# Kernel optimization log

Hardware: AMD Instinct MI355X
Metric: run time of the kernel (lower is better)

## Reference

```python
import jax, jax.numpy as jnp
import numpy as np

UNITS = 1024
NUM_HEADS = 8


def setup_inputs() -> dict:
    key = jax.random.key(0)
    k1, k2, k3 = jax.random.split(key, 3)
    B, S = 8, 1024
    memory = jax.random.normal(k1, (B, S, 2 * UNITS), dtype=jnp.float32)
    query = jax.random.normal(k2, (B, S, UNITS), dtype=jnp.float32)
    seq_mask = jax.random.randint(k3, (B, S), 0, 2, dtype=jnp.int32)
    b = jnp.zeros((1,), dtype=jnp.float32)  # learned scalar bias added to logits
    return {"memory": memory, "query": query, "seq_mask": seq_mask, "b": b}


def _split_heads(x, n):
    # [B, S, D] -> [B, n, S, D//n]
    B, S, D = x.shape
    return x.reshape(B, S, n, D // n).transpose(0, 2, 1, 3)


def reference(memory, query, seq_mask, b):
    H = NUM_HEADS
    depth = UNITS // H
    Q = _split_heads(query, H) * (depth ** -0.5)          # [B,H,S,d]
    k_mem, v_mem = jnp.split(memory, 2, axis=2)
    K = _split_heads(k_mem, H)                            # [B,H,S,d]
    V = _split_heads(v_mem, H)                            # [B,H,S,d]
    logits = jnp.einsum('bhqd,bhkd->bhqk', Q, K) + b[0]   # [B,H,S,S]
    mask = seq_mask.astype(jnp.float32)[:, None, None, :]  # [B,1,1,S]
    logits = logits + (-1e30) * (1.0 - mask)
    weights = jax.nn.softmax(logits, axis=-1)
    out = jnp.einsum('bhqk,bhkd->bhqd', weights, V)       # [B,H,S,d]
    B, _, S, _ = out.shape
    return out.transpose(0, 2, 1, 3).reshape(B, S, UNITS)
```

## Files before the change

### kernel.cpp

```cpp
#include <hip/hip_runtime.h>
#include <stdint.h>


typedef __attribute__((ext_vector_type(8))) short bf16x8;
typedef __attribute__((ext_vector_type(4))) float f32x4;
typedef __attribute__((ext_vector_type(16))) float f32x16;
typedef __attribute__((ext_vector_type(4))) unsigned int u32x4;

#define NB 8
#define SS 1024
#define NH 8
#define DH 128
#define BM 128
#define BN 64
#define KPAD 136
#define VPAD 72
#define NT (SS / BN)

__device__ __forceinline__ unsigned short f2bf(float f) {
    unsigned int u = __builtin_bit_cast(unsigned int, f);
    u += 0x7fffu + ((u >> 16) & 1u);
    return (unsigned short)(u >> 16);
}

__device__ __forceinline__ unsigned int cvt_pk_bf16(float lo, float hi) {
#if __has_builtin(__builtin_amdgcn_cvt_pk_bf16_f32)
    typedef __attribute__((ext_vector_type(2))) __bf16 bf16x2_t;
    bf16x2_t r = __builtin_amdgcn_cvt_pk_bf16_f32(lo, hi);
    return __builtin_bit_cast(unsigned int, r);
#else
    return (unsigned int)f2bf(lo) | ((unsigned int)f2bf(hi) << 16);
#endif
}

__device__ __forceinline__ void bar_lgkm() {
    asm volatile("s_waitcnt lgkmcnt(0)" ::: "memory");
    __builtin_amdgcn_s_barrier();
    asm volatile("" ::: "memory");
}

__device__ __forceinline__ void pswap(unsigned int &a, unsigned int &b) {
#if __has_builtin(__builtin_amdgcn_permlane32_swap)
    auto r = __builtin_amdgcn_permlane32_swap(a, b, false, false);
    a = (unsigned int)r[0];
    b = (unsigned int)r[1];
#else
    unsigned int sa = (unsigned int)__shfl_xor((int)a, 32, 64);
    unsigned int sb = (unsigned int)__shfl_xor((int)b, 32, 64);
    const bool hh = (threadIdx.x & 32) != 0;
    unsigned int na = hh ? sb : a;
    unsigned int nb = hh ? b : sa;
    a = na; b = nb;
#endif
}

__global__ __launch_bounds__(512, 4)
void attn_flash(const float* __restrict__ mem,
                const float* __restrict__ query,
                const int* __restrict__ seq_mask,
                float* __restrict__ out)
{
    __shared__ unsigned short K_lds[BN * KPAD];
    __shared__ unsigned short Vt_lds[DH * VPAD];

    const int tid  = threadIdx.x;
    const int wave = tid >> 6;
    const int lane = tid & 63;
    const int hi   = lane >> 5;
    const int l31  = lane & 31;
    const int wq   = wave & 3;
    const int wd   = wave >> 2;

    const int bh = blockIdx.x;
    const int b  = bh >> 3;
    const int h  = bh & 7;
    const int q0w = blockIdx.y * BM + wq * 32;

    bf16x8 qf[8];
    {
        const float* qb = query + ((size_t)(b * SS + q0w + l31) << 10) + h * DH + hi * 8;
        #pragma unroll
        for (int dep = 0; dep < 8; ++dep) {
            f32x4 lo = *(const f32x4*)(qb + dep * 16);
            f32x4 ho = *(const f32x4*)(qb + dep * 16 + 4);
            u32x4 q;
            q[0] = cvt_pk_bf16(lo[0], lo[1]);
            q[1] = cvt_pk_bf16(lo[2], lo[3]);
            q[2] = cvt_pk_bf16(ho[0], ho[1]);
            q[3] = cvt_pk_bf16(ho[2], ho[3]);
            qf[dep] = __builtin_bit_cast(bf16x8, q);
        }
    }

    f32x16 acc[2];
    #pragma unroll
    for (int dt = 0; dt < 2; ++dt)
        #pragma unroll
        for (int i = 0; i < 16; ++i) acc[dt][i] = 0.f;
    float l_i = 0.f;

    const float cs = 0.12752789747141537f;

    const int krow = tid >> 3;
    const int kcc  = (tid & 7) * 16;
    const int vq   = tid & 31;
    const int vg8  = tid >> 5;

    const float* kbase = mem + ((size_t)(b * SS) << 11) + h * DH;
    const float* vbase = kbase + 1024;
    const int* mbase = seq_mask + b * SS;

    int mv_cur = mbase[lane];
    int mv_nxt;

    for (int kt = 0; kt < NT; ++kt) {
        const int kk0 = kt * BN;

        bar_lgkm();

        {
            const float* src = kbase + ((size_t)(kk0 + krow) << 11) + kcc;
            f32x4 a0 = *(const f32x4*)src;
            f32x4 a1 = *(const f32x4*)(src + 4);
            f32x4 a2 = *(const f32x4*)(src + 8);
            f32x4 a3 = *(const f32x4*)(src + 12);
            u32x4 t0, t1;
            t0[0] = cvt_pk_bf16(a0[0], a0[1]);
            t0[1] = cvt_pk_bf16(a0[2], a0[3]);
            t0[2] = cvt_pk_bf16(a1[0], a1[1]);
            t0[3] = cvt_pk_bf16(a1[2], a1[3]);
            t1[0] = cvt_pk_bf16(a2[0], a2[1]);
            t1[1] = cvt_pk_bf16(a2[2], a2[3]);
            t1[2] = cvt_pk_bf16(a3[0], a3[1]);
            t1[3] = cvt_pk_bf16(a3[2], a3[3]);
            *(u32x4*)&K_lds[krow * KPAD + kcc] = t0;
            *(u32x4*)&K_lds[krow * KPAD + kcc + 8] = t1;
        }
        {
            const int d0 = vg8 * 8;
            const float* pa = vbase + ((size_t)(kk0 + 2 * vq) << 11) + d0;
            f32x4 a0 = *(const f32x4*)pa;
            f32x4 a1 = *(const f32x4*)(pa + 4);
            f32x4 b0 = *(const f32x4*)(pa + 2048);
            f32x4 b1 = *(const f32x4*)(pa + 2048 + 4);
            #pragma unroll
            for (int j = 0; j < 8; ++j) {
                float av = (j < 4) ? a0[j] : a1[j - 4];
                float bv = (j < 4) ? b0[j] : b1[j - 4];
                *(unsigned int*)&Vt_lds[(d0 + j) * VPAD + 2 * vq] =
                    cvt_pk_bf16(av, bv);
            }
        }

        const int kkn = (kt < NT - 1) ? kk0 + BN : kk0;
        mv_nxt = mbase[kkn + lane];

        bar_lgkm();

        const unsigned long long bmask = __ballot(mv_cur != 0);
        const unsigned int wsh0 = (unsigned int)(bmask >> (4 * hi));
        const unsigned int wsh1 = (unsigned int)(bmask >> (32 + 4 * hi));

        #pragma unroll
        for (int jt = 0; jt < 2; ++jt) {
            const unsigned int mword = jt ? wsh1 : wsh0;

            f32x16 s;
            #pragma unroll
            for (int i = 0; i < 16; ++i) s[i] = 0.f;
            __builtin_amdgcn_s_setprio(1);
            #pragma unroll
            for (int dep = 0; dep < 8; ++dep) {
                bf16x8 kf = *(const bf16x8*)&K_lds[(jt * 32 + l31) * KPAD + dep * 16 + hi * 8];
                s = __builtin_amdgcn_mfma_f32_32x32x16_bf16(kf, qf[dep], s, 0, 0, 0);
            }
            __builtin_amdgcn_s_setprio(0);

            float p[16];
            #pragma unroll
            for (int r = 0; r < 16; ++r) {
                const int sr = (r & 3) + 8 * (r >> 2);
                float e = __builtin_amdgcn_exp2f(s[r] * cs);
                p[r] = e * (float)((mword >> sr) & 1u);
            }
            {
                float t0 = (p[0] + p[1]) + (p[2] + p[3]);
                float t1 = (p[4] + p[5]) + (p[6] + p[7]);
                float t2 = (p[8] + p[9]) + (p[10] + p[11]);
                float t3 = (p[12] + p[13]) + (p[14] + p[15]);
                l_i += (t0 + t1) + (t2 + t3);
            }

            unsigned int w[8];
            #pragma unroll
            for (int i = 0; i < 8; ++i) w[i] = cvt_pk_bf16(p[2 * i], p[2 * i + 1]);
            pswap(w[0], w[2]); pswap(w[1], w[3]);
            pswap(w[4], w[6]); pswap(w[5], w[7]);
            bf16x8 af0 = __builtin_bit_cast(bf16x8, (u32x4){w[0], w[1], w[2], w[3]});
            bf16x8 af1 = __builtin_bit_cast(bf16x8, (u32x4){w[4], w[5], w[6], w[7]});

            __builtin_amdgcn_s_setprio(1);
            #pragma unroll
            for (int ksl = 0; ksl < 2; ++ksl) {
                bf16x8 ap = ksl ? af1 : af0;
                #pragma unroll
                for (int dt = 0; dt < 2; ++dt) {
                    bf16x8 bv = *(const bf16x8*)&Vt_lds[((wd * 2 + dt) * 32 + l31) * VPAD +
                                                        jt * 32 + ksl * 16 + hi * 8];
                    acc[dt] = __builtin_amdgcn_mfma_f32_32x32x16_bf16(ap, bv, acc[dt], 0, 0, 0);
                }
            }
            __builtin_amdgcn_s_setprio(0);
        }

        mv_cur = mv_nxt;
    }

    float lt = l_i + __shfl_xor(l_i, 32, 64);
    float invl = 1.f / lt;
    #pragma unroll
    for (int r = 0; r < 16; ++r) {
        const int qrow = (r & 3) + 8 * (r >> 2) + 4 * hi;
        float iv = __shfl(invl, qrow, 64);
        float* ob = out + ((size_t)(b * SS + q0w + qrow) << 10) + h * DH + wd * 64 + l31;
        ob[0]  = acc[0][r] * iv;
        ob[32] = acc[1][r] * iv;
    }
}

extern "C" void kernel_launch(void* const* d_in, const int* in_sizes, int n_in,
                              void* d_out, int out_size, void* d_ws, size_t ws_size,
                              hipStream_t stream)
{
    (void)in_sizes; (void)n_in; (void)d_ws; (void)ws_size; (void)out_size;
    const float* mem    = (const float*)d_in[0];
    const float* query  = (const float*)d_in[1];
    const int* seq_mask = (const int*)d_in[2];
    dim3 grid(NB * NH, SS / BM);
    attn_flash<<<grid, 512, 0, stream>>>(mem, query, seq_mask, (float*)d_out);
}
```

Baseline: 197.1 us.

## Split QK^T key columns across paired waves and exchange P through LDS

Before, each of the two waves sharing a query tile computed the full 64-key QK^T and softmax, duplicating that work. Now each wave computes only its 32-key half, writes its bf16 probabilities to a new LDS buffer, and reads its partner's half after an extra barrier to run the full PV product. Row sums are combined across the pair through LDS at the end. This halves QK MFMAs and exp work per wave, at the cost of one more block barrier per key tile plus LDS traffic.

```diff
diff --git a/kernel.cpp b/kernel.cpp
--- a/kernel.cpp
+++ b/kernel.cpp
@@ -62,6 +62,7 @@
 {
     __shared__ unsigned short K_lds[BN * KPAD];
     __shared__ unsigned short Vt_lds[DH * VPAD];
+    __shared__ __align__(16) unsigned char P_lds[2 * 8 * 64 * 16];
 
     const int tid  = threadIdx.x;
     const int wave = tid >> 6;
@@ -158,65 +159,76 @@
         bar_lgkm();
 
         const unsigned long long bmask = __ballot(mv_cur != 0);
-        const unsigned int wsh0 = (unsigned int)(bmask >> (4 * hi));
-        const unsigned int wsh1 = (unsigned int)(bmask >> (32 + 4 * hi));
-
-        #pragma unroll
-        for (int jt = 0; jt < 2; ++jt) {
-            const unsigned int mword = jt ? wsh1 : wsh0;
-
-            f32x16 s;
+        const unsigned int mword = (unsigned int)(bmask >> (wd * 32 + 4 * hi));
+
+        f32x16 s;
+        #pragma unroll
+        for (int i = 0; i < 16; ++i) s[i] = 0.f;
+        __builtin_amdgcn_s_setprio(1);
+        #pragma unroll
+        for (int dep = 0; dep < 8; ++dep) {
+            bf16x8 kf = *(const bf16x8*)&K_lds[(wd * 32 + l31) * KPAD + dep * 16 + hi * 8];
+            s = __builtin_amdgcn_mfma_f32_32x32x16_bf16(kf, qf[dep], s, 0, 0, 0);
+        }
+        __builtin_amdgcn_s_setprio(0);
+
+        float p[16];
+        #pragma unroll
+        for (int r = 0; r < 16; ++r) {
+            const int sr = (r & 3) + 8 * (r >> 2);
+            float e = __builtin_amdgcn_exp2f(s[r] * cs);
+            p[r] = e * (float)((mword >> sr) & 1u);
+        }
+        {
+            float t0 = (p[0] + p[1]) + (p[2] + p[3]);
+            float t1 = (p[4] + p[5]) + (p[6] + p[7]);
+            float t2 = (p[8] + p[9]) + (p[10] + p[11]);
+            float t3 = (p[12] + p[13]) + (p[14] + p[15]);
+            l_i += (t0 + t1) + (t2 + t3);
+        }
+
+        unsigned int w[8];
+        #pragma unroll
+        for (int i = 0; i < 8; ++i) w[i] = cvt_pk_bf16(p[2 * i], p[2 * i + 1]);
+        pswap(w[0], w[2]); pswap(w[1], w[3]);
+        pswap(w[4], w[6]); pswap(w[5], w[7]);
+        bf16x8 own0 = __builtin_bit_cast(bf16x8, (u32x4){w[0], w[1], w[2], w[3]});
+        bf16x8 own1 = __builtin_bit_cast(bf16x8, (u32x4){w[4], w[5], w[6], w[7]});
+
+        *(u32x4*)&P_lds[(0 * 512 + wave * 64 + lane) * 16] =
+            (u32x4){w[0], w[1], w[2], w[3]};
+        *(u32x4*)&P_lds[(1 * 512 + wave * 64 + lane) * 16] =
+            (u32x4){w[4], w[5], w[6], w[7]};
+
+        bar_lgkm();
+
+        const int pw = wave ^ 4;
+        bf16x8 paf0 = *(const bf16x8*)&P_lds[(0 * 512 + pw * 64 + lane) * 16];
+        bf16x8 paf1 = *(const bf16x8*)&P_lds[(1 * 512 + pw * 64 + lane) * 16];
+
+        __builtin_amdgcn_s_setprio(1);
+        #pragma unroll
+        for (int s4 = 0; s4 < 4; ++s4) {
+            bf16x8 ap = ((s4 >> 1) == wd) ? ((s4 & 1) ? own1 : own0)
+                                          : ((s4 & 1) ? paf1 : paf0);
             #pragma unroll
-            for (int i = 0; i < 16; ++i) s[i] = 0.f;
-            __builtin_amdgcn_s_setprio(1);
-            #pragma unroll
-            for (int dep = 0; dep < 8; ++dep) {
-                bf16x8 kf = *(const bf16x8*)&K_lds[(jt * 32 + l31) * KPAD + dep * 16 + hi * 8];
-                s = __builtin_amdgcn_mfma_f32_32x32x16_bf16(kf, qf[dep], s, 0, 0, 0);
+            for (int dt = 0; dt < 2; ++dt) {
+                bf16x8 bv = *(const bf16x8*)&Vt_lds[((wd * 2 + dt) * 32 + l31) * VPAD +
+                                                    s4 * 16 + hi * 8];
+                acc[dt] = __builtin_amdgcn_mfma_f32_32x32x16_bf16(ap, bv, acc[dt], 0, 0, 0);
             }
-            __builtin_amdgcn_s_setprio(0);
-
-            float p[16];
-            #pragma unroll
-            for (int r = 0; r < 16; ++r) {
-                const int sr = (r & 3) + 8 * (r >> 2);
-                float e = __builtin_amdgcn_exp2f(s[r] * cs);
-                p[r] = e * (float)((mword >> sr) & 1u);
-            }
-            {
-                float t0 = (p[0] + p[1]) + (p[2] + p[3]);
-                float t1 = (p[4] + p[5]) + (p[6] + p[7]);
-                float t2 = (p[8] + p[9]) + (p[10] + p[11]);
-                float t3 = (p[12] + p[13]) + (p[14] + p[15]);
-                l_i += (t0 + t1) + (t2 + t3);
-            }
-
-            unsigned int w[8];
-            #pragma unroll
-            for (int i = 0; i < 8; ++i) w[i] = cvt_pk_bf16(p[2 * i], p[2 * i + 1]);
-            pswap(w[0], w[2]); pswap(w[1], w[3]);
-            pswap(w[4], w[6]); pswap(w[5], w[7]);
-            bf16x8 af0 = __builtin_bit_cast(bf16x8, (u32x4){w[0], w[1], w[2], w[3]});
-            bf16x8 af1 = __builtin_bit_cast(bf16x8, (u32x4){w[4], w[5], w[6], w[7]});
-
-            __builtin_amdgcn_s_setprio(1);
-            #pragma unroll
-            for (int ksl = 0; ksl < 2; ++ksl) {
-                bf16x8 ap = ksl ? af1 : af0;
-                #pragma unroll
-                for (int dt = 0; dt < 2; ++dt) {
-                    bf16x8 bv = *(const bf16x8*)&Vt_lds[((wd * 2 + dt) * 32 + l31) * VPAD +
-                                                        jt * 32 + ksl * 16 + hi * 8];
-                    acc[dt] = __builtin_amdgcn_mfma_f32_32x32x16_bf16(ap, bv, acc[dt], 0, 0, 0);
-                }
-            }
-            __builtin_amdgcn_s_setprio(0);
-        }
+        }
+        __builtin_amdgcn_s_setprio(0);
 
         mv_cur = mv_nxt;
     }
 
-    float lt = l_i + __shfl_xor(l_i, 32, 64);
+    float hl = l_i + __shfl_xor(l_i, 32, 64);
+    __syncthreads();
+    float* scr_l = (float*)P_lds;
+    scr_l[wave * 64 + lane] = hl;
+    __syncthreads();
+    float lt = hl + scr_l[(wave ^ 4) * 64 + lane];
     float invl = 1.f / lt;
     #pragma unroll
     for (int r = 0; r < 16; ++r) {
```

New measurement: 180.8 us. 1.09x faster.
